# Performance work log

Measured on AMD Instinct MI355X. Metric: run time of the kernel, lower is better.

The kernel has to match this reference:

```python
import jax, jax.numpy as jnp
import numpy as np

INIT_STDEV = 0.01

def setup_inputs() -> dict:
    key = jax.random.key(0)
    k1, k2, k3 = jax.random.split(key, 3)
    B, S, D = 8, 4096, 768
    x = jax.random.normal(k1, (B, S, D), dtype=jnp.float32)
    att_v = jax.random.normal(k2, (D,), dtype=jnp.float32) * INIT_STDEV
    att_W = jax.random.normal(k3, (D, D), dtype=jnp.float32) * INIT_STDEV
    return {"x": x, "att_v": att_v, "att_W": att_W}

def reference(x, att_v, att_W):
    # y = x @ W : [B,S,D]; scores = tanh(y) . v over D : [B,S]
    y = jnp.tanh(jnp.einsum('bsd,de->bse', x, att_W))
    scores = jnp.einsum('bsd,d->bs', y, att_v)
    weights = jax.nn.softmax(scores, axis=-1)            # softmax over sequence
    out = jnp.einsum('bs,bsd->bd', weights, x)           # attsum pool
    return out.astype(jnp.float32)
```

## Files before the change

kernel.cpp:

```cpp
#include <hip/hip_runtime.h>
#include <hip/hip_bf16.h>

constexpr int Bb = 8;
constexpr int Ss = 4096;
constexpr int Dd = 768;
constexpr int Mm = Bb * Ss;

typedef __bf16 bf16x8 __attribute__((ext_vector_type(8)));
typedef __bf16 bf16x4 __attribute__((ext_vector_type(4)));
typedef float f32x4 __attribute__((ext_vector_type(4)));

__device__ __forceinline__ float fast_tanh(float x) {
    return 1.f - 2.f / (__expf(2.f * x) + 1.f);
}

__device__ __forceinline__ void load_lds16(const void* g, void* l) {
    __builtin_amdgcn_global_load_lds(
        (const __attribute__((address_space(1))) unsigned int*)g,
        (__attribute__((address_space(3))) unsigned int*)l, 16, 0, 0);
}

__global__ __launch_bounds__(256) void convW(const float* __restrict__ W,
                                             __bf16* __restrict__ Wt) {
    __shared__ float tile[32][33];
    const int tx = threadIdx.x & 31;
    const int ty = threadIdx.x >> 5;
    const int kb = blockIdx.x * 32;
    const int nb = blockIdx.y * 32;
#pragma unroll
    for (int i = 0; i < 32; i += 8)
        tile[ty + i][tx] = W[(size_t)(kb + ty + i) * Dd + nb + tx];
    __syncthreads();
#pragma unroll
    for (int i = 0; i < 32; i += 8)
        Wt[(size_t)(nb + ty + i) * Dd + kb + tx] = (__bf16)tile[tx][ty + i];
}

__global__ __launch_bounds__(512, 4) void scores_gemm(
    const float* __restrict__ x, const __bf16* __restrict__ Wt,
    const float* __restrict__ v, float* __restrict__ scores) {
    __shared__ __bf16 As[2][64 * 32];
    __shared__ __bf16 Bs[2][384 * 32];
    __shared__ float ssc[8][32];

    const int t = threadIdx.x;
    const int nb = blockIdx.x;
    const int mb = blockIdx.y;
    const int lane = t & 63;
    const int wave = t >> 6;
    const int wm = wave >> 2;
    const int wn = wave & 3;
    const int quad = lane >> 4;
    const int lid = lane & 15;

    const int arow = t >> 3;
    const int ac4 = t & 7;
    const float* agp = x + (size_t)(mb * 64 + arow) * Dd + ac4 * 4;

    const __bf16* bg[3];
    int bl[3];
#pragma unroll
    for (int j = 0; j < 3; ++j) {
        const int flat = j * 8192 + t * 16;
        const int col = flat >> 6;
        const int off = flat & 63;
        bg[j] = Wt + (size_t)(nb * 384 + col) * Dd + (off >> 1);
        bl[j] = flat >> 1;
    }

    f32x4 acc[2][6];
#pragma unroll
    for (int tm = 0; tm < 2; ++tm)
#pragma unroll
        for (int nt = 0; nt < 6; ++nt) acc[tm][nt] = (f32x4){0.f, 0.f, 0.f, 0.f};

    {
        const float4 a = *(const float4*)(agp);
        bf16x4 p;
        p[0] = (__bf16)a.x; p[1] = (__bf16)a.y; p[2] = (__bf16)a.z; p[3] = (__bf16)a.w;
        *(bf16x4*)(&As[0][arow * 32 + ac4 * 4]) = p;
#pragma unroll
        for (int j = 0; j < 3; ++j) load_lds16(bg[j], &Bs[0][bl[j]]);
    }

    for (int kb = 0; kb < 24; ++kb) {
        const int p = kb & 1;
        __syncthreads();

        float4 an;
        if (kb < 23) {
            an = *(const float4*)(agp + (kb + 1) * 32);
#pragma unroll
            for (int j = 0; j < 3; ++j)
                load_lds16(bg[j] + (kb + 1) * 32, &Bs[1 - p][bl[j]]);
        }

        bf16x8 af[2], bfr[6];
#pragma unroll
        for (int tm = 0; tm < 2; ++tm)
            af[tm] = *(const bf16x8*)(&As[p][(wm * 32 + tm * 16 + lid) * 32 + quad * 8]);
#pragma unroll
        for (int nt = 0; nt < 6; ++nt)
            bfr[nt] = *(const bf16x8*)(&Bs[p][(wn * 96 + nt * 16 + lid) * 32 + quad * 8]);

#pragma unroll
        for (int tm = 0; tm < 2; ++tm)
#pragma unroll
            for (int nt = 0; nt < 6; ++nt)
                acc[tm][nt] = __builtin_amdgcn_mfma_f32_16x16x32_bf16(af[tm], bfr[nt], acc[tm][nt], 0, 0, 0);

        if (kb < 23) {
            bf16x4 pa;
            pa[0] = (__bf16)an.x; pa[1] = (__bf16)an.y;
            pa[2] = (__bf16)an.z; pa[3] = (__bf16)an.w;
            *(bf16x4*)(&As[1 - p][arow * 32 + ac4 * 4]) = pa;
        }
    }

    float vv[6];
#pragma unroll
    for (int nt = 0; nt < 6; ++nt)
        vv[nt] = v[nb * 384 + wn * 96 + nt * 16 + lid];

#pragma unroll
    for (int tm = 0; tm < 2; ++tm)
#pragma unroll
        for (int r = 0; r < 4; ++r) {
            float s = 0.f;
#pragma unroll
            for (int nt = 0; nt < 6; ++nt) s += vv[nt] * fast_tanh(acc[tm][nt][r]);
            s += __shfl_xor(s, 1);
            s += __shfl_xor(s, 2);
            s += __shfl_xor(s, 4);
            s += __shfl_xor(s, 8);
            if (lid == 0) ssc[wave][tm * 16 + quad * 4 + r] = s;
        }
    __syncthreads();
    if (t < 64) {
        const int wmh = t >> 5;
        const int rl = t & 31;
        float s = 0.f;
#pragma unroll
        for (int ww = 0; ww < 4; ++ww) s += ssc[wmh * 4 + ww][rl];
        atomicAdd(&scores[mb * 64 + t], s);
    }
}

__global__ __launch_bounds__(256) void softmax_k(const float* __restrict__ scores,
                                                 float* __restrict__ weights) {
    const int b = blockIdx.x;
    const int t = threadIdx.x;
    const float* s = scores + (size_t)b * Ss;
    float* wgt = weights + (size_t)b * Ss;
    __shared__ float red[256];

    float mx = -1e30f;
    for (int i = t; i < Ss; i += 256) mx = fmaxf(mx, s[i]);
    red[t] = mx;
    __syncthreads();
    for (int o = 128; o > 0; o >>= 1) {
        if (t < o) red[t] = fmaxf(red[t], red[t + o]);
        __syncthreads();
    }
    mx = red[0];
    __syncthreads();
    float sum = 0.f;
    for (int i = t; i < Ss; i += 256) {
        const float e = __expf(s[i] - mx);
        wgt[i] = e;
        sum += e;
    }
    red[t] = sum;
    __syncthreads();
    for (int o = 128; o > 0; o >>= 1) {
        if (t < o) red[t] += red[t + o];
        __syncthreads();
    }
    const float inv = 1.f / red[0];
    for (int i = t; i < Ss; i += 256) wgt[i] *= inv;
}

__global__ __launch_bounds__(192) void pool1(const float* __restrict__ x,
                                             const float* __restrict__ weights,
                                             float* __restrict__ partial) {
    const int b = blockIdx.y;
    const int c = blockIdx.x;
    const int t = threadIdx.x;
    const float* base = x + ((size_t)b * Ss + c * 32) * Dd;
    const float* wrow = weights + (size_t)b * Ss + c * 32;
    float4 acc = make_float4(0.f, 0.f, 0.f, 0.f);
#pragma unroll 8
    for (int i = 0; i < 32; ++i) {
        const float ww = wrow[i];
        const float4 xv = *(const float4*)(base + (size_t)i * Dd + t * 4);
        acc.x += ww * xv.x;
        acc.y += ww * xv.y;
        acc.z += ww * xv.z;
        acc.w += ww * xv.w;
    }
    *(float4*)(partial + ((size_t)(b * 128 + c)) * Dd + t * 4) = acc;
}

__global__ __launch_bounds__(768) void pool2(const float* __restrict__ partial,
                                             float* __restrict__ out) {
    const int b = blockIdx.x;
    const int d = threadIdx.x;
    float s = 0.f;
#pragma unroll 8
    for (int c = 0; c < 128; ++c) s += partial[((size_t)(b * 128 + c)) * Dd + d];
    out[(size_t)b * Dd + d] = s;
}

extern "C" void kernel_launch(void* const* d_in, const int* in_sizes, int n_in,
                              void* d_out, int out_size, void* d_ws, size_t ws_size,
                              hipStream_t stream) {
    (void)in_sizes; (void)n_in; (void)ws_size; (void)out_size;
    const float* x = (const float*)d_in[0];
    const float* v = (const float*)d_in[1];
    const float* W = (const float*)d_in[2];

    char* ws = (char*)d_ws;
    __bf16* Wt = (__bf16*)ws;
    float* scores = (float*)(ws + 1179648);
    float* weights = (float*)(ws + 1179648 + 131072);
    float* partial = (float*)(ws + 1179648 + 262144);

    hipMemsetAsync(scores, 0, Mm * sizeof(float), stream);

    convW<<<dim3(Dd / 32, Dd / 32), 256, 0, stream>>>(W, Wt);
    scores_gemm<<<dim3(2, Mm / 64), 512, 0, stream>>>(x, Wt, v, scores);
    softmax_k<<<dim3(Bb), 256, 0, stream>>>(scores, weights);
    pool1<<<dim3(128, Bb), 192, 0, stream>>>(x, weights, partial);
    pool2<<<dim3(Bb), 768, 0, stream>>>(partial, (float*)d_out);
}
```

Before: 240.8 us.

## Retile scores GEMM to 128x256 blocks with XOR-swizzled LDS layout

Changes the GEMM tile from 64x384 to 128x256 per block, giving each wave a 4x4 grid of MFMA tiles instead of 2x6. This raises operand reuse per LDS read and halves how often x is re-read across N blocks relative to M. It also adds an XOR swizzle on the k-slot, applied both in the bf16 W transpose and in the A/B LDS writes and reads, to reduce LDS bank conflicts. The cost is three N blocks per row tile, so more passes over x, and a different register footprint.

```diff
diff --git a/kernel.cpp b/kernel.cpp
--- a/kernel.cpp
+++ b/kernel.cpp
@@ -32,16 +32,19 @@
         tile[ty + i][tx] = W[(size_t)(kb + ty + i) * Dd + nb + tx];
     __syncthreads();
 #pragma unroll
-    for (int i = 0; i < 32; i += 8)
-        Wt[(size_t)(nb + ty + i) * Dd + kb + tx] = (__bf16)tile[tx][ty + i];
+    for (int i = 0; i < 32; i += 8) {
+        const int n = nb + ty + i;
+        const int txs = (tx & 7) | ((((tx >> 3) & 3) ^ ((n >> 1) & 3)) << 3);
+        Wt[(size_t)n * Dd + kb + txs] = (__bf16)tile[tx][ty + i];
+    }
 }
 
 __global__ __launch_bounds__(512, 4) void scores_gemm(
     const float* __restrict__ x, const __bf16* __restrict__ Wt,
     const float* __restrict__ v, float* __restrict__ scores) {
-    __shared__ __bf16 As[2][64 * 32];
-    __shared__ __bf16 Bs[2][384 * 32];
-    __shared__ float ssc[8][32];
+    __shared__ __bf16 As[2][128 * 32];
+    __shared__ __bf16 Bs[2][256 * 32];
+    __shared__ float ssc[8][64];
 
     const int t = threadIdx.x;
     const int nb = blockIdx.x;
@@ -52,83 +55,88 @@
     const int wn = wave & 3;
     const int quad = lane >> 4;
     const int lid = lane & 15;
-
-    const int arow = t >> 3;
-    const int ac4 = t & 7;
-    const float* agp = x + (size_t)(mb * 64 + arow) * Dd + ac4 * 4;
-
-    const __bf16* bg[3];
-    int bl[3];
-#pragma unroll
-    for (int j = 0; j < 3; ++j) {
+    const int rslot = ((quad ^ ((lid >> 1) & 3)) * 8);
+
+    const int arow = t >> 2;
+    const int aslotraw = t & 3;
+    const int aslot = aslotraw ^ ((arow >> 1) & 3);
+    const float* agp = x + (size_t)(mb * 128 + arow) * Dd + aslotraw * 8;
+    const int awr = arow * 32 + aslot * 8;
+
+    const __bf16* bg[2];
+    int bl[2];
+#pragma unroll
+    for (int j = 0; j < 2; ++j) {
         const int flat = j * 8192 + t * 16;
         const int col = flat >> 6;
-        const int off = flat & 63;
-        bg[j] = Wt + (size_t)(nb * 384 + col) * Dd + (off >> 1);
+        bg[j] = Wt + (size_t)(nb * 256 + col) * Dd + ((flat & 63) >> 1);
         bl[j] = flat >> 1;
     }
 
-    f32x4 acc[2][6];
-#pragma unroll
-    for (int tm = 0; tm < 2; ++tm)
-#pragma unroll
-        for (int nt = 0; nt < 6; ++nt) acc[tm][nt] = (f32x4){0.f, 0.f, 0.f, 0.f};
+    f32x4 acc[4][4];
+#pragma unroll
+    for (int tm = 0; tm < 4; ++tm)
+#pragma unroll
+        for (int nt = 0; nt < 4; ++nt) acc[tm][nt] = (f32x4){0.f, 0.f, 0.f, 0.f};
 
     {
-        const float4 a = *(const float4*)(agp);
-        bf16x4 p;
-        p[0] = (__bf16)a.x; p[1] = (__bf16)a.y; p[2] = (__bf16)a.z; p[3] = (__bf16)a.w;
-        *(bf16x4*)(&As[0][arow * 32 + ac4 * 4]) = p;
-#pragma unroll
-        for (int j = 0; j < 3; ++j) load_lds16(bg[j], &Bs[0][bl[j]]);
+        const float4 a0 = *(const float4*)(agp);
+        const float4 a1 = *(const float4*)(agp + 4);
+        bf16x8 pa;
+        pa[0] = (__bf16)a0.x; pa[1] = (__bf16)a0.y; pa[2] = (__bf16)a0.z; pa[3] = (__bf16)a0.w;
+        pa[4] = (__bf16)a1.x; pa[5] = (__bf16)a1.y; pa[6] = (__bf16)a1.z; pa[7] = (__bf16)a1.w;
+        *(bf16x8*)(&As[0][awr]) = pa;
+#pragma unroll
+        for (int j = 0; j < 2; ++j) load_lds16(bg[j], &Bs[0][bl[j]]);
     }
 
     for (int kb = 0; kb < 24; ++kb) {
         const int p = kb & 1;
         __syncthreads();
 
-        float4 an;
+        float4 a0n, a1n;
         if (kb < 23) {
-            an = *(const float4*)(agp + (kb + 1) * 32);
-#pragma unroll
-            for (int j = 0; j < 3; ++j)
+            a0n = *(const float4*)(agp + (kb + 1) * 32);
+            a1n = *(const float4*)(agp + (kb + 1) * 32 + 4);
+#pragma unroll
+            for (int j = 0; j < 2; ++j)
                 load_lds16(bg[j] + (kb + 1) * 32, &Bs[1 - p][bl[j]]);
         }
 
-        bf16x8 af[2], bfr[6];
-#pragma unroll
-        for (int tm = 0; tm < 2; ++tm)
-            af[tm] = *(const bf16x8*)(&As[p][(wm * 32 + tm * 16 + lid) * 32 + quad * 8]);
-#pragma unroll
-        for (int nt = 0; nt < 6; ++nt)
-            bfr[nt] = *(const bf16x8*)(&Bs[p][(wn * 96 + nt * 16 + lid) * 32 + quad * 8]);
-
-#pragma unroll
-        for (int tm = 0; tm < 2; ++tm)
-#pragma unroll
-            for (int nt = 0; nt < 6; ++nt)
+        bf16x8 af[4], bfr[4];
+#pragma unroll
+        for (int tm = 0; tm < 4; ++tm)
+            af[tm] = *(const bf16x8*)(&As[p][(wm * 64 + tm * 16 + lid) * 32 + rslot]);
+#pragma unroll
+        for (int nt = 0; nt < 4; ++nt)
+            bfr[nt] = *(const bf16x8*)(&Bs[p][(wn * 64 + nt * 16 + lid) * 32 + rslot]);
+
+#pragma unroll
+        for (int tm = 0; tm < 4; ++tm)
+#pragma unroll
+            for (int nt = 0; nt < 4; ++nt)
                 acc[tm][nt] = __builtin_amdgcn_mfma_f32_16x16x32_bf16(af[tm], bfr[nt], acc[tm][nt], 0, 0, 0);
 
         if (kb < 23) {
-            bf16x4 pa;
-            pa[0] = (__bf16)an.x; pa[1] = (__bf16)an.y;
-            pa[2] = (__bf16)an.z; pa[3] = (__bf16)an.w;
-            *(bf16x4*)(&As[1 - p][arow * 32 + ac4 * 4]) = pa;
+            bf16x8 pa;
+            pa[0] = (__bf16)a0n.x; pa[1] = (__bf16)a0n.y; pa[2] = (__bf16)a0n.z; pa[3] = (__bf16)a0n.w;
+            pa[4] = (__bf16)a1n.x; pa[5] = (__bf16)a1n.y; pa[6] = (__bf16)a1n.z; pa[7] = (__bf16)a1n.w;
+            *(bf16x8*)(&As[1 - p][awr]) = pa;
         }
     }
 
-    float vv[6];
-#pragma unroll
-    for (int nt = 0; nt < 6; ++nt)
-        vv[nt] = v[nb * 384 + wn * 96 + nt * 16 + lid];
-
-#pragma unroll
-    for (int tm = 0; tm < 2; ++tm)
+    float vv[4];
+#pragma unroll
+    for (int nt = 0; nt < 4; ++nt)
+        vv[nt] = v[nb * 256 + wn * 64 + nt * 16 + lid];
+
+#pragma unroll
+    for (int tm = 0; tm < 4; ++tm)
 #pragma unroll
         for (int r = 0; r < 4; ++r) {
             float s = 0.f;
 #pragma unroll
-            for (int nt = 0; nt < 6; ++nt) s += vv[nt] * fast_tanh(acc[tm][nt][r]);
+            for (int nt = 0; nt < 4; ++nt) s += vv[nt] * fast_tanh(acc[tm][nt][r]);
             s += __shfl_xor(s, 1);
             s += __shfl_xor(s, 2);
             s += __shfl_xor(s, 4);
@@ -136,13 +144,13 @@
             if (lid == 0) ssc[wave][tm * 16 + quad * 4 + r] = s;
         }
     __syncthreads();
-    if (t < 64) {
-        const int wmh = t >> 5;
-        const int rl = t & 31;
+    if (t < 128) {
+        const int wmh = t >> 6;
+        const int rl = t & 63;
         float s = 0.f;
 #pragma unroll
         for (int ww = 0; ww < 4; ++ww) s += ssc[wmh * 4 + ww][rl];
-        atomicAdd(&scores[mb * 64 + t], s);
+        atomicAdd(&scores[mb * 128 + t], s);
     }
 }
 
@@ -228,7 +236,7 @@
     hipMemsetAsync(scores, 0, Mm * sizeof(float), stream);
 
     convW<<<dim3(Dd / 32, Dd / 32), 256, 0, stream>>>(W, Wt);
-    scores_gemm<<<dim3(2, Mm / 64), 512, 0, stream>>>(x, Wt, v, scores);
+    scores_gemm<<<dim3(3, Mm / 128), 512, 0, stream>>>(x, Wt, v, scores);
     softmax_k<<<dim3(Bb), 256, 0, stream>>>(scores, weights);
     pool1<<<dim3(128, Bb), 192, 0, stream>>>(x, weights, partial);
     pool2<<<dim3(Bb), 768, 0, stream>>>(partial, (float*)d_out);
```

Result: no change. 238.9 us (-0.8%).
